# Kernel optimization log

Measured on AMD Instinct MI355X. Metric: run time of the kernel, lower is better.

## Reference

```python
import jax, jax.numpy as jnp
import numpy as np

BATCH, SEQ, HIDDEN = 8, 4096, 1024

def setup_inputs() -> dict:
    key = jax.random.key(0)
    hidden_states = jax.random.normal(key, (BATCH, SEQ, HIDDEN), dtype=jnp.float32)
    return {"hidden_states": hidden_states}

def reference(hidden_states) -> jnp.ndarray:
    # FFT along the sequence axis with orthonormal normalization (1/sqrt(N)),
    # then keep only the real part (FNet-style Fourier token mixing).
    fft_out = jnp.fft.fft(hidden_states, axis=1, norm="ortho")
    return jnp.real(fft_out).astype(hidden_states.dtype)
```

## Files before the change

### kernel.cpp

```cpp
#include <hip/hip_runtime.h>
#include <hip/hip_fp16.h>


static constexpr int SEQ = 4096;
static constexpr int HID = 1024;

struct alignas(8) h2x2 { __half2 a, b; };

__device__ __forceinline__ int rev4_3(int r) {
    return ((r & 3) << 4) | (r & 12) | ((r >> 4) & 3);
}

template <int MC>
__device__ __forceinline__ void fft64_lds(float* re, float* im, int off, int stride, int mbase) {
    #pragma unroll
    for (int s = 0; s < 3; ++s) {
        const int L = 1 << (2 * s);
        const float ang = -6.283185307179586f / (float)(4 * L);
        #pragma unroll
        for (int mi = 0; mi < MC; ++mi) {
            const int m  = mbase + mi;
            const int j  = m & (L - 1);
            const int i0 = ((m >> (2 * s)) << (2 * s + 2)) + j;
            const int a0 = (i0        ) * stride + off;
            const int a1 = (i0 +     L) * stride + off;
            const int a2 = (i0 + 2 * L) * stride + off;
            const int a3 = (i0 + 3 * L) * stride + off;
            const float e0x = re[a0], e0y = im[a0];
            const float e1x = re[a1], e1y = im[a1];
            const float e2x = re[a2], e2y = im[a2];
            const float e3x = re[a3], e3y = im[a3];
            float w1s, w1c;
            __sincosf(ang * (float)j, &w1s, &w1c);
            const float w2c = w1c * w1c - w1s * w1s, w2s = 2.f * w1c * w1s;
            const float w3c = w2c * w1c - w2s * w1s, w3s = w2c * w1s + w2s * w1c;
            const float t1x = e1x * w1c - e1y * w1s, t1y = e1x * w1s + e1y * w1c;
            const float t2x = e2x * w2c - e2y * w2s, t2y = e2x * w2s + e2y * w2c;
            const float t3x = e3x * w3c - e3y * w3s, t3y = e3x * w3s + e3y * w3c;
            const float a02x = e0x + t2x, a02y = e0y + t2y;
            const float s02x = e0x - t2x, s02y = e0y - t2y;
            const float a13x = t1x + t3x, a13y = t1y + t3y;
            const float s13x = t1x - t3x, s13y = t1y - t3y;
            re[a0] = a02x + a13x;  im[a0] = a02y + a13y;
            re[a1] = s02x + s13y;  im[a1] = s02y - s13x;
            re[a2] = a02x - a13x;  im[a2] = a02y - a13y;
            re[a3] = s02x - s13y;  im[a3] = s02y + s13x;
        }
        __syncthreads();
    }
}


__global__ __launch_bounds__(256) void fft_pass1_h(const float* __restrict__ x,
                                                   __half2* __restrict__ u) {
    __shared__ float sre[64 * 33];
    __shared__ float sim[64 * 33];
    const int t  = threadIdx.x;
    const int pc = blockIdx.x & 15;
    const int n2 = (blockIdx.x >> 4) & 63;
    const int b  = blockIdx.x >> 10;
    const float* xb = x + (size_t)b * SEQ * HID + pc * 64;
    __half2*     ub = u + (size_t)b * SEQ * 512 + pc * 32;

    const int c  = t & 15;
    const int r0 = t >> 4;
    #pragma unroll
    for (int i = 0; i < 4; ++i) {
        const int r  = r0 + 16 * i;
        const float4 f = *(const float4*)(xb + (size_t)(n2 + 64 * r) * HID + 4 * c);
        const int rr = rev4_3(r);
        sre[rr * 33 + 2 * c]     = f.x;  sim[rr * 33 + 2 * c]     = f.y;
        sre[rr * 33 + 2 * c + 1] = f.z;  sim[rr * 33 + 2 * c + 1] = f.w;
    }
    __syncthreads();

    fft64_lds<2>(sre, sim, t & 31, 33, 2 * (t >> 5));

    const float tw = -1.5339807878856412e-3f;
    const float sc = 0.015625f;
    #pragma unroll
    for (int i = 0; i < 4; ++i) {
        const int k1 = r0 + 16 * i;
        float ws, wc;
        __sincosf(tw * (float)(n2 * k1), &ws, &wc);
        wc *= sc;  ws *= sc;
        const float ar = sre[k1 * 33 + 2 * c],     ai = sim[k1 * 33 + 2 * c];
        const float br = sre[k1 * 33 + 2 * c + 1], bi = sim[k1 * 33 + 2 * c + 1];
        h2x2 o;
        o.a = __floats2half2_rn(ar * wc - ai * ws, ar * ws + ai * wc);
        o.b = __floats2half2_rn(br * wc - bi * ws, br * ws + bi * wc);
        *(h2x2*)(ub + (size_t)(64 * n2 + k1) * 512 + 2 * c) = o;
    }
}

__global__ __launch_bounds__(256) void fft_pass2_h(const __half2* __restrict__ u,
                                                   float* __restrict__ out) {
    __shared__ float lds[4352];
    const int t   = threadIdx.x;
    const int b   = blockIdx.x >> 10;
    const int idx = blockIdx.x & 1023;
    const __half2* ub = u   + (size_t)b * SEQ * 512;
    float*         ob = out + (size_t)b * SEQ * HID;
    const float scale = 0.5f;

    if (idx < 992) {
        const int k1 = 1 + (idx >> 5);
        const int pc = idx & 31;
        float* are = lds;          float* aim = lds + 1088;
        float* bre = lds + 2176;   float* bim = lds + 3264;
        const int c  = t & 7;
        const int rg = t >> 3;
        #pragma unroll
        for (int i = 0; i < 2; ++i) {
            const int n2 = rg + 32 * i;
            const int rr = rev4_3(n2);
            const h2x2 va = *(const h2x2*)(ub + (size_t)(64 * n2 + k1)      * 512 + pc * 16 + 2 * c);
            const h2x2 vb = *(const h2x2*)(ub + (size_t)(64 * n2 + 64 - k1) * 512 + pc * 16 + 2 * c);
            const float2 a0 = __half22float2(va.a), a1 = __half22float2(va.b);
            const float2 b0 = __half22float2(vb.a), b1 = __half22float2(vb.b);
            are[rr * 17 + 2 * c]     = a0.x;  aim[rr * 17 + 2 * c]     = a0.y;
            are[rr * 17 + 2 * c + 1] = a1.x;  aim[rr * 17 + 2 * c + 1] = a1.y;
            bre[rr * 17 + 2 * c]     = b0.x;  bim[rr * 17 + 2 * c]     = b0.y;
            bre[rr * 17 + 2 * c + 1] = b1.x;  bim[rr * 17 + 2 * c + 1] = b1.y;
        }
        __syncthreads();

        float* fre = lds + (t >> 7) * 2176;
        fft64_lds<2>(fre, fre + 1088, t & 15, 17, 2 * ((t >> 4) & 7));

        #pragma unroll
        for (int i = 0; i < 2; ++i) {
            const int k2 = rg + 32 * i;
            const int q  = 63 - k2;
            float4 f, g;
            f.x = (are[k2 * 17 + 2 * c]     + bre[q * 17 + 2 * c])     * scale;
            f.y = (aim[k2 * 17 + 2 * c]     + bim[q * 17 + 2 * c])     * scale;
            f.z = (are[k2 * 17 + 2 * c + 1] + bre[q * 17 + 2 * c + 1]) * scale;
            f.w = (aim[k2 * 17 + 2 * c + 1] + bim[q * 17 + 2 * c + 1]) * scale;
            *(float4*)(ob + (size_t)(k1 + 64 * k2)      * HID + pc * 32 + 4 * c) = f;
            g.x = (bre[k2 * 17 + 2 * c]     + are[q * 17 + 2 * c])     * scale;
            g.y = (bim[k2 * 17 + 2 * c]     + aim[q * 17 + 2 * c])     * scale;
            g.z = (bre[k2 * 17 + 2 * c + 1] + are[q * 17 + 2 * c + 1]) * scale;
            g.w = (bim[k2 * 17 + 2 * c + 1] + aim[q * 17 + 2 * c + 1]) * scale;
            *(float4*)(ob + (size_t)(64 - k1 + 64 * k2) * HID + pc * 32 + 4 * c) = g;
        }
    } else {
        const int s  = idx - 992;
        const int k1 = (s >> 4) * 32;
        const int pc = s & 15;
        float* sre = lds;
        float* sim = lds + 2112;
        const int c  = t & 15;
        const int rg = t >> 4;
        #pragma unroll
        for (int i = 0; i < 4; ++i) {
            const int n2 = rg + 16 * i;
            const int rr = rev4_3(n2);
            const h2x2 v = *(const h2x2*)(ub + (size_t)(64 * n2 + k1) * 512 + pc * 32 + 2 * c);
            const float2 p0 = __half22float2(v.a), p1 = __half22float2(v.b);
            sre[rr * 33 + 2 * c]     = p0.x;  sim[rr * 33 + 2 * c]     = p0.y;
            sre[rr * 33 + 2 * c + 1] = p1.x;  sim[rr * 33 + 2 * c + 1] = p1.y;
        }
        __syncthreads();

        fft64_lds<2>(sre, sim, t & 31, 33, 2 * (t >> 5));

        #pragma unroll
        for (int i = 0; i < 4; ++i) {
            const int k2 = rg + 16 * i;
            const int q  = (k1 == 0) ? ((64 - k2) & 63) : (63 - k2);
            float4 f;
            f.x = (sre[k2 * 33 + 2 * c]     + sre[q * 33 + 2 * c])     * scale;
            f.y = (sim[k2 * 33 + 2 * c]     + sim[q * 33 + 2 * c])     * scale;
            f.z = (sre[k2 * 33 + 2 * c + 1] + sre[q * 33 + 2 * c + 1]) * scale;
            f.w = (sim[k2 * 33 + 2 * c + 1] + sim[q * 33 + 2 * c + 1]) * scale;
            *(float4*)(ob + (size_t)(k1 + 64 * k2) * HID + pc * 64 + 4 * c) = f;
        }
    }
}


__global__ __launch_bounds__(256) void fft_pass1(const float* __restrict__ x,
                                                 float* __restrict__ out) {
    __shared__ float sre[64 * 65];
    __shared__ float sim[64 * 65];
    const int t  = threadIdx.x;
    const int pc = blockIdx.x & 7;
    const int n2 = (blockIdx.x >> 3) & 63;
    const int b  = blockIdx.x >> 9;
    const float* xb = x   + (size_t)b * SEQ * HID + pc * 128;
    float*       ob = out + (size_t)b * SEQ * HID + pc * 128;

    const int c  = t & 31;
    const int r0 = t >> 5;
    #pragma unroll
    for (int i = 0; i < 8; ++i) {
        const int r  = r0 + 8 * i;
        const float4 f = *(const float4*)(xb + (size_t)(n2 + 64 * r) * HID + 4 * c);
        const int rr = rev4_3(r);
        sre[rr * 65 + 2 * c]     = f.x;  sim[rr * 65 + 2 * c]     = f.y;
        sre[rr * 65 + 2 * c + 1] = f.z;  sim[rr * 65 + 2 * c + 1] = f.w;
    }
    __syncthreads();

    fft64_lds<4>(sre, sim, t & 63, 65, 4 * (t >> 6));

    const float tw = -1.5339807878856412e-3f;
    #pragma unroll
    for (int i = 0; i < 8; ++i) {
        const int k1 = r0 + 8 * i;
        float ws, wc;
        __sincosf(tw * (float)(n2 * k1), &ws, &wc);
        const float ar = sre[k1 * 65 + 2 * c],     ai = sim[k1 * 65 + 2 * c];
        const float br = sre[k1 * 65 + 2 * c + 1], bi = sim[k1 * 65 + 2 * c + 1];
        float4 f;
        f.x = ar * wc - ai * ws;  f.y = ar * ws + ai * wc;
        f.z = br * wc - bi * ws;  f.w = br * ws + bi * wc;
        *(float4*)(ob + (size_t)(64 * n2 + k1) * HID + 4 * c) = f;
    }
}

__global__ __launch_bounds__(256) void fft_pass2(float* out) {
    __shared__ float lds[8448];
    const int t   = threadIdx.x;
    const int b   = blockIdx.x >> 9;
    const int idx = blockIdx.x & 511;
    float* ob = out + (size_t)b * SEQ * HID;
    const float scale = 1.0f / 128.0f;

    if (idx < 496) {
        const int k1 = 1 + (idx >> 4);
        const int pc = idx & 15;
        float* are = lds;          float* aim = lds + 2112;
        float* bre = lds + 4224;   float* bim = lds + 6336;
        const int c  = t & 15;
        const int rg = t >> 4;
        #pragma unroll
        for (int i = 0; i < 4; ++i) {
            const int n2 = rg + 16 * i;
            const int rr = rev4_3(n2);
            const float4 fa = *(const float4*)(ob + (size_t)(64 * n2 + k1)      * HID + pc * 64 + 4 * c);
            const float4 fb = *(const float4*)(ob + (size_t)(64 * n2 + 64 - k1) * HID + pc * 64 + 4 * c);
            are[rr * 33 + 2 * c]     = fa.x;  aim[rr * 33 + 2 * c]     = fa.y;
            are[rr * 33 + 2 * c + 1] = fa.z;  aim[rr * 33 + 2 * c + 1] = fa.w;
            bre[rr * 33 + 2 * c]     = fb.x;  bim[rr * 33 + 2 * c]     = fb.y;
            bre[rr * 33 + 2 * c + 1] = fb.z;  bim[rr * 33 + 2 * c + 1] = fb.w;
        }
        __syncthreads();

        const int lane = t & 63;
        float* fre = lds + 4224 * (lane >> 5);
        fft64_lds<4>(fre, fre + 2112, lane & 31, 33, 4 * (t >> 6));

        #pragma unroll
        for (int i = 0; i < 4; ++i) {
            const int k2 = rg + 16 * i;
            const int q  = 63 - k2;
            float4 f, g;
            f.x = (are[k2 * 33 + 2 * c]     + bre[q * 33 + 2 * c])     * scale;
            f.y = (aim[k2 * 33 + 2 * c]     + bim[q * 33 + 2 * c])     * scale;
            f.z = (are[k2 * 33 + 2 * c + 1] + bre[q * 33 + 2 * c + 1]) * scale;
            f.w = (aim[k2 * 33 + 2 * c + 1] + bim[q * 33 + 2 * c + 1]) * scale;
            *(float4*)(ob + (size_t)(k1 + 64 * k2)      * HID + pc * 64 + 4 * c) = f;
            g.x = (bre[k2 * 33 + 2 * c]     + are[q * 33 + 2 * c])     * scale;
            g.y = (bim[k2 * 33 + 2 * c]     + aim[q * 33 + 2 * c])     * scale;
            g.z = (bre[k2 * 33 + 2 * c + 1] + are[q * 33 + 2 * c + 1]) * scale;
            g.w = (bim[k2 * 33 + 2 * c + 1] + aim[q * 33 + 2 * c + 1]) * scale;
            *(float4*)(ob + (size_t)(64 - k1 + 64 * k2) * HID + pc * 64 + 4 * c) = g;
        }
    } else {
        const int s  = idx - 496;
        const int k1 = (s >> 3) * 32;
        const int pc = s & 7;
        float* sre = lds;
        float* sim = lds + 4160;
        const int c  = t & 31;
        const int rg = t >> 5;
        #pragma unroll
        for (int i = 0; i < 8; ++i) {
            const int n2 = rg + 8 * i;
            const int rr = rev4_3(n2);
            const float4 f = *(const float4*)(ob + (size_t)(64 * n2 + k1) * HID + pc * 128 + 4 * c);
            sre[rr * 65 + 2 * c]     = f.x;  sim[rr * 65 + 2 * c]     = f.y;
            sre[rr * 65 + 2 * c + 1] = f.z;  sim[rr * 65 + 2 * c + 1] = f.w;
        }
        __syncthreads();

        fft64_lds<4>(sre, sim, t & 63, 65, 4 * (t >> 6));

        #pragma unroll
        for (int i = 0; i < 8; ++i) {
            const int k2 = rg + 8 * i;
            const int q  = (k1 == 0) ? ((64 - k2) & 63) : (63 - k2);
            float4 f;
            f.x = (sre[k2 * 65 + 2 * c]     + sre[q * 65 + 2 * c])     * scale;
            f.y = (sim[k2 * 65 + 2 * c]     + sim[q * 65 + 2 * c])     * scale;
            f.z = (sre[k2 * 65 + 2 * c + 1] + sre[q * 65 + 2 * c + 1]) * scale;
            f.w = (sim[k2 * 65 + 2 * c + 1] + sim[q * 65 + 2 * c + 1]) * scale;
            *(float4*)(ob + (size_t)(k1 + 64 * k2) * HID + pc * 128 + 4 * c) = f;
        }
    }
}

extern "C" void kernel_launch(void* const* d_in, const int* in_sizes, int n_in,
                              void* d_out, int out_size, void* d_ws, size_t ws_size,
                              hipStream_t stream) {
    const float* x = (const float*)d_in[0];
    float* out = (float*)d_out;
    const size_t need = (size_t)8 * SEQ * 512 * sizeof(__half2);
    if (ws_size >= need) {
        __half2* u = (__half2*)d_ws;
        fft_pass1_h<<<dim3(8 * 64 * 16), dim3(256), 0, stream>>>(x, u);
        fft_pass2_h<<<dim3(8 * 1024), dim3(256), 0, stream>>>(u, out);
    } else {
        fft_pass1<<<dim3(8 * 64 * 8), dim3(256), 0, stream>>>(x, out);
        fft_pass2<<<dim3(8 * 512), dim3(256), 0, stream>>>(out);
    }
}
```

Measured before the change: 262.7 us.

## Replace LDS radix-4 FFT-64 with register radix-8 two-stage FFT

Both passes now compute each 64-point FFT as two register-resident radix-8 butterflies with a single LDS transpose between them, replacing three LDS-based radix-4 stages, each followed by a barrier. Twiddles are generated by complex-multiply recurrence chains instead of one sincos per element. Global accesses become per-thread float2/half2 loads spread across 8 rows, which changes coalescing width. The aim is to cut LDS traffic and synchronisation while keeping the fp16 intermediate.

```diff
diff --git a/kernel.cpp b/kernel.cpp
--- a/kernel.cpp
+++ b/kernel.cpp
@@ -10,6 +10,215 @@
 __device__ __forceinline__ int rev4_3(int r) {
     return ((r & 3) << 4) | (r & 12) | ((r >> 4) & 3);
 }
+
+
+__device__ __forceinline__ void fft8(float* xr, float* xi) {
+    const float C = 0.70710678118654752f;
+    float ar[8], ai[8];
+    ar[0] = xr[0] + xr[4];  ai[0] = xi[0] + xi[4];
+    ar[1] = xr[0] - xr[4];  ai[1] = xi[0] - xi[4];
+    ar[2] = xr[2] + xr[6];  ai[2] = xi[2] + xi[6];
+    ar[3] = xr[2] - xr[6];  ai[3] = xi[2] - xi[6];
+    ar[4] = xr[1] + xr[5];  ai[4] = xi[1] + xi[5];
+    ar[5] = xr[1] - xr[5];  ai[5] = xi[1] - xi[5];
+    ar[6] = xr[3] + xr[7];  ai[6] = xi[3] + xi[7];
+    ar[7] = xr[3] - xr[7];  ai[7] = xi[3] - xi[7];
+    float br[8], bi[8];
+    br[0] = ar[0] + ar[2];  bi[0] = ai[0] + ai[2];
+    br[2] = ar[0] - ar[2];  bi[2] = ai[0] - ai[2];
+    br[1] = ar[1] + ai[3];  bi[1] = ai[1] - ar[3];
+    br[3] = ar[1] - ai[3];  bi[3] = ai[1] + ar[3];
+    br[4] = ar[4] + ar[6];  bi[4] = ai[4] + ai[6];
+    br[6] = ar[4] - ar[6];  bi[6] = ai[4] - ai[6];
+    br[5] = ar[5] + ai[7];  bi[5] = ai[5] - ar[7];
+    br[7] = ar[5] - ai[7];  bi[7] = ai[5] + ar[7];
+    const float t0r = br[4],                 t0i = bi[4];
+    const float t1r = C * (br[5] + bi[5]),   t1i = C * (bi[5] - br[5]);
+    const float t2r = bi[6],                 t2i = -br[6];
+    const float t3r = C * (bi[7] - br[7]),   t3i = -C * (br[7] + bi[7]);
+    xr[0] = br[0] + t0r;  xi[0] = bi[0] + t0i;
+    xr[4] = br[0] - t0r;  xi[4] = bi[0] - t0i;
+    xr[1] = br[1] + t1r;  xi[1] = bi[1] + t1i;
+    xr[5] = br[1] - t1r;  xi[5] = bi[1] - t1i;
+    xr[2] = br[2] + t2r;  xi[2] = bi[2] + t2i;
+    xr[6] = br[2] - t2r;  xi[6] = bi[2] - t2i;
+    xr[3] = br[3] + t3r;  xi[3] = bi[3] + t3i;
+    xr[7] = br[3] - t3r;  xi[7] = bi[3] - t3i;
+}
+
+__device__ __forceinline__ void twiddle_chain(float* xr, float* xi,
+                                              const float wc, const float ws) {
+    float cr = wc, ci = ws;
+    #pragma unroll
+    for (int k = 1; k < 8; ++k) {
+        const float tr = xr[k] * cr - xi[k] * ci;
+        xi[k] = xr[k] * ci + xi[k] * cr;
+        xr[k] = tr;
+        if (k < 7) {
+            const float nr = cr * wc - ci * ws;
+            const float ni = cr * ws + ci * wc;
+            cr = nr;  ci = ni;
+        }
+    }
+}
+
+
+__global__ __launch_bounds__(256) void fft_pass1_r8(const float* __restrict__ x,
+                                                    __half2* __restrict__ u) {
+    __shared__ float2 zs[2112];
+    const int t  = threadIdx.x;
+    const int pc = blockIdx.x & 15;
+    const int n2 = (blockIdx.x >> 4) & 63;
+    const int b  = blockIdx.x >> 10;
+    const int c  = t & 31;
+    const int q  = t >> 5;
+
+    const float* xb = x + (size_t)b * SEQ * HID + (size_t)(pc * 64 + 2 * c);
+    float xr[8], xi[8];
+    #pragma unroll
+    for (int a = 0; a < 8; ++a) {
+        const float2 v = *(const float2*)(xb + (size_t)(n2 + 64 * (8 * a + q)) * HID);
+        xr[a] = v.x;  xi[a] = v.y;
+    }
+    fft8(xr, xi);
+    {
+        float wsn, wcs;
+        __sincosf(-0.09817477042468103f * (float)q, &wsn, &wcs);
+        twiddle_chain(xr, xi, wcs, wsn);
+    }
+    #pragma unroll
+    for (int k = 0; k < 8; ++k)
+        zs[(k * 8 + q) * 33 + c] = make_float2(xr[k], xi[k]);
+    __syncthreads();
+    #pragma unroll
+    for (int r = 0; r < 8; ++r) {
+        const float2 v = zs[(q * 8 + r) * 33 + c];
+        xr[r] = v.x;  xi[r] = v.y;
+    }
+    fft8(xr, xi);
+
+    const float tw = -1.5339807878856412e-3f;
+    float w0c, w0s, wsc, wss;
+    __sincosf(tw * (float)(n2 * q), &w0s, &w0c);
+    __sincosf(tw * (float)(n2 * 8), &wss, &wsc);
+    const float sc = 0.015625f;
+    w0c *= sc;  w0s *= sc;
+    __half2* ub = u + (size_t)b * SEQ * 512 + (size_t)(64 * n2 + q) * 512 + pc * 32 + c;
+    #pragma unroll
+    for (int kh = 0; kh < 8; ++kh) {
+        const float orr = xr[kh] * w0c - xi[kh] * w0s;
+        const float oii = xr[kh] * w0s + xi[kh] * w0c;
+        ub[(size_t)(8 * kh) * 512] = __floats2half2_rn(orr, oii);
+        if (kh < 7) {
+            const float nc = w0c * wsc - w0s * wss;
+            const float ns = w0c * wss + w0s * wsc;
+            w0c = nc;  w0s = ns;
+        }
+    }
+}
+
+__global__ __launch_bounds__(256) void fft_pass2_r8(const __half2* __restrict__ u,
+                                                    float* __restrict__ out) {
+    __shared__ float2 vs[2176];
+    const int t   = threadIdx.x;
+    const int b   = blockIdx.x >> 10;
+    const int idx = blockIdx.x & 1023;
+    const __half2* ub = u   + (size_t)b * SEQ * 512;
+    float*         ob = out + (size_t)b * SEQ * HID;
+    const float scale = 0.5f;
+    float xr[8], xi[8];
+
+    if (idx < 992) {
+        const int k1 = 1 + (idx >> 5);
+        const int pc = idx & 31;
+        const int ab = t >> 7;
+        const int q  = (t >> 4) & 7;
+        const int c  = t & 15;
+        const int k1sel = ab ? 64 - k1 : k1;
+        const int p  = pc * 16 + c;
+        const __half2* up = ub + (size_t)k1sel * 512 + p;
+        #pragma unroll
+        for (int a = 0; a < 8; ++a) {
+            const float2 v = __half22float2(up[(size_t)(64 * (8 * a + q)) * 512]);
+            xr[a] = v.x;  xi[a] = v.y;
+        }
+        fft8(xr, xi);
+        {
+            float wsn, wcs;
+            __sincosf(-0.09817477042468103f * (float)q, &wsn, &wcs);
+            twiddle_chain(xr, xi, wcs, wsn);
+        }
+        const int base = ab * 64;
+        #pragma unroll
+        for (int k = 0; k < 8; ++k)
+            vs[(base + k * 8 + q) * 17 + c] = make_float2(xr[k], xi[k]);
+        __syncthreads();
+        #pragma unroll
+        for (int r = 0; r < 8; ++r) {
+            const float2 v = vs[(base + q * 8 + r) * 17 + c];
+            xr[r] = v.x;  xi[r] = v.y;
+        }
+        fft8(xr, xi);
+        __syncthreads();
+        #pragma unroll
+        for (int k = 0; k < 8; ++k)
+            vs[(base + k * 8 + q) * 17 + c] = make_float2(xr[k], xi[k]);
+        __syncthreads();
+        float* op = ob + (size_t)k1sel * HID + 2 * p;
+        #pragma unroll
+        for (int kh = 0; kh < 8; ++kh) {
+            const float2 pv = vs[((64 - base) + (7 - kh) * 8 + (7 - q)) * 17 + c];
+            const int k2 = q + 8 * kh;
+            *(float2*)(op + (size_t)(64 * k2) * HID) =
+                make_float2((xr[kh] + pv.x) * scale, (xi[kh] + pv.y) * scale);
+        }
+    } else {
+        const int s  = idx - 992;
+        const int k1 = (s >> 4) * 32;
+        const int pc = s & 15;
+        const int q  = t >> 5;
+        const int c  = t & 31;
+        const int p  = pc * 32 + c;
+        const __half2* up = ub + (size_t)k1 * 512 + p;
+        #pragma unroll
+        for (int a = 0; a < 8; ++a) {
+            const float2 v = __half22float2(up[(size_t)(64 * (8 * a + q)) * 512]);
+            xr[a] = v.x;  xi[a] = v.y;
+        }
+        fft8(xr, xi);
+        {
+            float wsn, wcs;
+            __sincosf(-0.09817477042468103f * (float)q, &wsn, &wcs);
+            twiddle_chain(xr, xi, wcs, wsn);
+        }
+        #pragma unroll
+        for (int k = 0; k < 8; ++k)
+            vs[(k * 8 + q) * 33 + c] = make_float2(xr[k], xi[k]);
+        __syncthreads();
+        #pragma unroll
+        for (int r = 0; r < 8; ++r) {
+            const float2 v = vs[(q * 8 + r) * 33 + c];
+            xr[r] = v.x;  xi[r] = v.y;
+        }
+        fft8(xr, xi);
+        __syncthreads();
+        #pragma unroll
+        for (int k = 0; k < 8; ++k)
+            vs[(k * 8 + q) * 33 + c] = make_float2(xr[k], xi[k]);
+        __syncthreads();
+        const int q2 = (k1 == 0) ? ((8 - q) & 7) : (7 - q);
+        float* op = ob + (size_t)k1 * HID + 2 * p;
+        #pragma unroll
+        for (int kh = 0; kh < 8; ++kh) {
+            const int kh2 = (k1 == 0 && q == 0) ? ((8 - kh) & 7) : (7 - kh);
+            const float2 pv = vs[(kh2 * 8 + q2) * 33 + c];
+            const int k2 = q + 8 * kh;
+            *(float2*)(op + (size_t)(64 * k2) * HID) =
+                make_float2((xr[kh] + pv.x) * scale, (xi[kh] + pv.y) * scale);
+        }
+    }
+}
+
 
 template <int MC>
 __device__ __forceinline__ void fft64_lds(float* re, float* im, int off, int stride, int mbase) {
@@ -50,136 +259,6 @@
     }
 }
 
-
-__global__ __launch_bounds__(256) void fft_pass1_h(const float* __restrict__ x,
-                                                   __half2* __restrict__ u) {
-    __shared__ float sre[64 * 33];
-    __shared__ float sim[64 * 33];
-    const int t  = threadIdx.x;
-    const int pc = blockIdx.x & 15;
-    const int n2 = (blockIdx.x >> 4) & 63;
-    const int b  = blockIdx.x >> 10;
-    const float* xb = x + (size_t)b * SEQ * HID + pc * 64;
-    __half2*     ub = u + (size_t)b * SEQ * 512 + pc * 32;
-
-    const int c  = t & 15;
-    const int r0 = t >> 4;
-    #pragma unroll
-    for (int i = 0; i < 4; ++i) {
-        const int r  = r0 + 16 * i;
-        const float4 f = *(const float4*)(xb + (size_t)(n2 + 64 * r) * HID + 4 * c);
-        const int rr = rev4_3(r);
-        sre[rr * 33 + 2 * c]     = f.x;  sim[rr * 33 + 2 * c]     = f.y;
-        sre[rr * 33 + 2 * c + 1] = f.z;  sim[rr * 33 + 2 * c + 1] = f.w;
-    }
-    __syncthreads();
-
-    fft64_lds<2>(sre, sim, t & 31, 33, 2 * (t >> 5));
-
-    const float tw = -1.5339807878856412e-3f;
-    const float sc = 0.015625f;
-    #pragma unroll
-    for (int i = 0; i < 4; ++i) {
-        const int k1 = r0 + 16 * i;
-        float ws, wc;
-        __sincosf(tw * (float)(n2 * k1), &ws, &wc);
-        wc *= sc;  ws *= sc;
-        const float ar = sre[k1 * 33 + 2 * c],     ai = sim[k1 * 33 + 2 * c];
-        const float br = sre[k1 * 33 + 2 * c + 1], bi = sim[k1 * 33 + 2 * c + 1];
-        h2x2 o;
-        o.a = __floats2half2_rn(ar * wc - ai * ws, ar * ws + ai * wc);
-        o.b = __floats2half2_rn(br * wc - bi * ws, br * ws + bi * wc);
-        *(h2x2*)(ub + (size_t)(64 * n2 + k1) * 512 + 2 * c) = o;
-    }
-}
-
-__global__ __launch_bounds__(256) void fft_pass2_h(const __half2* __restrict__ u,
-                                                   float* __restrict__ out) {
-    __shared__ float lds[4352];
-    const int t   = threadIdx.x;
-    const int b   = blockIdx.x >> 10;
-    const int idx = blockIdx.x & 1023;
-    const __half2* ub = u   + (size_t)b * SEQ * 512;
-    float*         ob = out + (size_t)b * SEQ * HID;
-    const float scale = 0.5f;
-
-    if (idx < 992) {
-        const int k1 = 1 + (idx >> 5);
-        const int pc = idx & 31;
-        float* are = lds;          float* aim = lds + 1088;
-        float* bre = lds + 2176;   float* bim = lds + 3264;
-        const int c  = t & 7;
-        const int rg = t >> 3;
-        #pragma unroll
-        for (int i = 0; i < 2; ++i) {
-            const int n2 = rg + 32 * i;
-            const int rr = rev4_3(n2);
-            const h2x2 va = *(const h2x2*)(ub + (size_t)(64 * n2 + k1)      * 512 + pc * 16 + 2 * c);
-            const h2x2 vb = *(const h2x2*)(ub + (size_t)(64 * n2 + 64 - k1) * 512 + pc * 16 + 2 * c);
-            const float2 a0 = __half22float2(va.a), a1 = __half22float2(va.b);
-            const float2 b0 = __half22float2(vb.a), b1 = __half22float2(vb.b);
-            are[rr * 17 + 2 * c]     = a0.x;  aim[rr * 17 + 2 * c]     = a0.y;
-            are[rr * 17 + 2 * c + 1] = a1.x;  aim[rr * 17 + 2 * c + 1] = a1.y;
-            bre[rr * 17 + 2 * c]     = b0.x;  bim[rr * 17 + 2 * c]     = b0.y;
-            bre[rr * 17 + 2 * c + 1] = b1.x;  bim[rr * 17 + 2 * c + 1] = b1.y;
-        }
-        __syncthreads();
-
-        float* fre = lds + (t >> 7) * 2176;
-        fft64_lds<2>(fre, fre + 1088, t & 15, 17, 2 * ((t >> 4) & 7));
-
-        #pragma unroll
-        for (int i = 0; i < 2; ++i) {
-            const int k2 = rg + 32 * i;
-            const int q  = 63 - k2;
-            float4 f, g;
-            f.x = (are[k2 * 17 + 2 * c]     + bre[q * 17 + 2 * c])     * scale;
-            f.y = (aim[k2 * 17 + 2 * c]     + bim[q * 17 + 2 * c])     * scale;
-            f.z = (are[k2 * 17 + 2 * c + 1] + bre[q * 17 + 2 * c + 1]) * scale;
-            f.w = (aim[k2 * 17 + 2 * c + 1] + bim[q * 17 + 2 * c + 1]) * scale;
-            *(float4*)(ob + (size_t)(k1 + 64 * k2)      * HID + pc * 32 + 4 * c) = f;
-            g.x = (bre[k2 * 17 + 2 * c]     + are[q * 17 + 2 * c])     * scale;
-            g.y = (bim[k2 * 17 + 2 * c]     + aim[q * 17 + 2 * c])     * scale;
-            g.z = (bre[k2 * 17 + 2 * c + 1] + are[q * 17 + 2 * c + 1]) * scale;
-            g.w = (bim[k2 * 17 + 2 * c + 1] + aim[q * 17 + 2 * c + 1]) * scale;
-            *(float4*)(ob + (size_t)(64 - k1 + 64 * k2) * HID + pc * 32 + 4 * c) = g;
-        }
-    } else {
-        const int s  = idx - 992;
-        const int k1 = (s >> 4) * 32;
-        const int pc = s & 15;
-        float* sre = lds;
-        float* sim = lds + 2112;
-        const int c  = t & 15;
-        const int rg = t >> 4;
-        #pragma unroll
-        for (int i = 0; i < 4; ++i) {
-            const int n2 = rg + 16 * i;
-            const int rr = rev4_3(n2);
-            const h2x2 v = *(const h2x2*)(ub + (size_t)(64 * n2 + k1) * 512 + pc * 32 + 2 * c);
-            const float2 p0 = __half22float2(v.a), p1 = __half22float2(v.b);
-            sre[rr * 33 + 2 * c]     = p0.x;  sim[rr * 33 + 2 * c]     = p0.y;
-            sre[rr * 33 + 2 * c + 1] = p1.x;  sim[rr * 33 + 2 * c + 1] = p1.y;
-        }
-        __syncthreads();
-
-        fft64_lds<2>(sre, sim, t & 31, 33, 2 * (t >> 5));
-
-        #pragma unroll
-        for (int i = 0; i < 4; ++i) {
-            const int k2 = rg + 16 * i;
-            const int q  = (k1 == 0) ? ((64 - k2) & 63) : (63 - k2);
-            float4 f;
-            f.x = (sre[k2 * 33 + 2 * c]     + sre[q * 33 + 2 * c])     * scale;
-            f.y = (sim[k2 * 33 + 2 * c]     + sim[q * 33 + 2 * c])     * scale;
-            f.z = (sre[k2 * 33 + 2 * c + 1] + sre[q * 33 + 2 * c + 1]) * scale;
-            f.w = (sim[k2 * 33 + 2 * c + 1] + sim[q * 33 + 2 * c + 1]) * scale;
-            *(float4*)(ob + (size_t)(k1 + 64 * k2) * HID + pc * 64 + 4 * c) = f;
-        }
-    }
-}
-
-
 __global__ __launch_bounds__(256) void fft_pass1(const float* __restrict__ x,
                                                  float* __restrict__ out) {
     __shared__ float sre[64 * 65];
@@ -310,8 +389,8 @@
     const size_t need = (size_t)8 * SEQ * 512 * sizeof(__half2);
     if (ws_size >= need) {
         __half2* u = (__half2*)d_ws;
-        fft_pass1_h<<<dim3(8 * 64 * 16), dim3(256), 0, stream>>>(x, u);
-        fft_pass2_h<<<dim3(8 * 1024), dim3(256), 0, stream>>>(u, out);
+        fft_pass1_r8<<<dim3(8 * 64 * 16), dim3(256), 0, stream>>>(x, u);
+        fft_pass2_r8<<<dim3(8 * 1024), dim3(256), 0, stream>>>(u, out);
     } else {
         fft_pass1<<<dim3(8 * 64 * 8), dim3(256), 0, stream>>>(x, out);
         fft_pass2<<<dim3(8 * 512), dim3(256), 0, stream>>>(out);
```

Measured after the change: 263.9 us. About the same (+0.5%).
